# Optimization experiments

Hardware: AMD Instinct MI355X
Metric: run time of the kernel (lower is better)

## Reference

```python
import jax, jax.numpy as jnp
import numpy as np

NUM_EMBEDDINGS = 8192
EMA_DECAY = 0.99


def setup_inputs() -> dict:
    key = jax.random.key(0)
    k1, k2 = jax.random.split(key)
    encodings = jax.random.normal(k1, (16, 128, 32, 32), dtype=jnp.float32)
    weight = 0.02 * jax.random.normal(k2, (NUM_EMBEDDINGS, 128), dtype=jnp.float32)
    return {"encodings": encodings, "weight": weight}


def reference(encodings, weight):
    B, C, H, W = encodings.shape
    K = weight.shape[0]
    # [B, C, H, W] -> [N, C], N = B*H*W
    x = encodings.transpose(0, 2, 3, 1).reshape(-1, C)
    # pairwise squared distances via norms + matmul: [N, K]
    dist = (
        jnp.sum(x * x, axis=1, keepdims=True)
        + jnp.sum(weight * weight, axis=1)[None, :]
        - 2.0 * jnp.matmul(x, weight.T)
    )
    quantized_ids = jnp.argmin(dist, axis=1)  # [N] int
    # straight-through estimator
    q = x + jax.lax.stop_gradient(weight[quantized_ids] - x)  # [N, C]
    # training-mode EMA codebook update (scatter-add counts and sums)
    counts = jax.ops.segment_sum(
        jnp.ones((x.shape[0],), dtype=x.dtype), quantized_ids, num_segments=K
    )
    sums = jax.ops.segment_sum(x, quantized_ids, num_segments=K)
    new_means = sums / (counts[:, None] + 1e-12)
    new_weight = EMA_DECAY * weight + (1.0 - EMA_DECAY) * new_means
    ids_out = quantized_ids.reshape(B, H, W)
    q_out = q.reshape(B, H, W, C).transpose(0, 3, 1, 2)  # [B, C, H, W]
    return ids_out, q_out, new_weight
```

## Files before the change

kernel.cpp:

```cpp
#include <hip/hip_runtime.h>
#include <stdint.h>
#include <stddef.h>


#define N_ROWS   16384
#define K_CODES  8192
#define C_DIM    128

typedef _Float16 f16x8 __attribute__((ext_vector_type(8)));
typedef float    f32x4 __attribute__((ext_vector_type(4)));

__global__ __launch_bounds__(256) void prep(const float* __restrict__ enc,
                                            const float* __restrict__ w,
                                            _Float16* __restrict__ Ap,
                                            _Float16* __restrict__ Bp,
                                            float* __restrict__ xT,
                                            float* __restrict__ xnorm,
                                            float* __restrict__ wnorm,
                                            float* __restrict__ wnmax128) {
  __shared__ float t[128][65];
  const int tid = threadIdx.x;
  if (blockIdx.x < 256) {
    const int b = blockIdx.x >> 4;
    const int hw0 = (blockIdx.x & 15) << 6;
    #pragma unroll
    for (int i = 0; i < 32; ++i) {
      int idx = i * 256 + tid;
      int c = idx >> 6, hwl = idx & 63;
      t[c][hwl] = enc[((size_t)(b * 128 + c) << 10) + hw0 + hwl];
    }
    __syncthreads();
    const int r = tid >> 2, sub = tid & 3;
    const int n = (b << 10) + hw0 + r;
    const int R = n >> 4, m = n & 15;
    float s = 0.f;
    #pragma unroll
    for (int q = 0; q < 4; ++q) {
      f16x8 hv;
      float vv[8];
      #pragma unroll
      for (int e = 0; e < 8; ++e) {
        float v = t[sub * 32 + q * 8 + e][r];
        vv[e] = v;
        s += v * v;
        hv[e] = (_Float16)v;
      }
      *(f16x8*)(Ap + ((size_t)(R * 4 + sub) * 64 + (m + 16 * q)) * 8) = hv;
      *(float4*)(xT + (size_t)n * 128 + sub * 32 + q * 8) =
          (float4){vv[0], vv[1], vv[2], vv[3]};
      *(float4*)(xT + (size_t)n * 128 + sub * 32 + q * 8 + 4) =
          (float4){vv[4], vv[5], vv[6], vv[7]};
    }
    s += __shfl_xor(s, 1);
    s += __shfl_xor(s, 2);
    if (sub == 0) xnorm[n] = s;
  } else {
    __shared__ float wred[4];
    const int kk = (blockIdx.x - 256) * 64 + (tid >> 2), sub = tid & 3;
    const int R = kk >> 4, m = kk & 15;
    const float* base = w + (size_t)kk * C_DIM + sub * 32;
    float s = 0.f;
    #pragma unroll
    for (int q = 0; q < 4; ++q) {
      f16x8 hv;
      float4 va = *(const float4*)(base + q * 8);
      float4 vb = *(const float4*)(base + q * 8 + 4);
      float vv[8] = {va.x, va.y, va.z, va.w, vb.x, vb.y, vb.z, vb.w};
      #pragma unroll
      for (int e = 0; e < 8; ++e) { s += vv[e] * vv[e]; hv[e] = (_Float16)vv[e]; }
      *(f16x8*)(Bp + ((size_t)(R * 4 + sub) * 64 + (m + 16 * q)) * 8) = hv;
    }
    s += __shfl_xor(s, 1);
    s += __shfl_xor(s, 2);
    if (sub == 0) wnorm[kk] = s;
    float wx = s;
    #pragma unroll
    for (int st = 1; st <= 32; st <<= 1) wx = fmaxf(wx, __shfl_xor(wx, st));
    if ((tid & 63) == 0) wred[tid >> 6] = wx;
    __syncthreads();
    if (tid == 0)
      wnmax128[blockIdx.x - 256] =
          fmaxf(fmaxf(wred[0], wred[1]), fmaxf(wred[2], wred[3]));
  }
}

__global__ __launch_bounds__(512) void gemm_argmin(
    const _Float16* __restrict__ Ap, const _Float16* __restrict__ Bp,
    const float* __restrict__ wnorm,
    float* __restrict__ pd1, float* __restrict__ pd2,
    unsigned* __restrict__ icount, unsigned* __restrict__ fcount)
{
  __shared__ _Float16 sbuf[2][16384];
  const int tid = threadIdx.x;
  const int lane = tid & 63, wave = tid >> 6;
  const int m = lane & 15, q = lane >> 4;
  const int cs = blockIdx.x;
  const int row0 = blockIdx.y * 128;
  const int Tr = blockIdx.y * 8 + wave;

  if (cs == 0 && blockIdx.y == 0 && tid == 0) {
    *icount = 0u; *fcount = 0u;
  }

#define STAGE(b, itn) do {                                                   \
    const size_t bh_ = ((size_t)((cs * 64 + (itn) * 8) * 4) << 9);           \
    _Pragma("unroll")                                                        \
    for (int r_ = 0; r_ < 4; ++r_) {                                         \
      __builtin_amdgcn_global_load_lds(                                      \
          (const __attribute__((address_space(1))) void*)                    \
              (Bp + bh_ + ((size_t)(r_ * 512 + tid) << 3)),                  \
          (__attribute__((address_space(3))) void*)                          \
              (&sbuf[b][(r_ * 512 + tid) << 3]),                             \
          16, 0, 0);                                                         \
    }                                                                        \
  } while (0)

  f16x8 bx[4];
  #pragma unroll
  for (int kc = 0; kc < 4; ++kc)
    bx[kc] = *(const f16x8*)(Ap + (((size_t)Tr * 4 + kc) << 9) + (lane << 3));
  const int row = row0 + wave * 16 + m;
  const unsigned q5 = (unsigned)(q << 5);

  STAGE(0, 0);

  for (int it = 0; it < 8; ++it) {
    __syncthreads();
    if (it < 7) STAGE((it + 1) & 1, it + 1);
    const _Float16* fb = &sbuf[it & 1][0];
    const int T0 = cs * 64 + it * 8;
    const int g = cs * 8 + it;
    f32x4 acc[8];
    #pragma unroll
    for (int tj = 0; tj < 8; ++tj) acc[tj] = (f32x4){0.f, 0.f, 0.f, 0.f};
    #pragma unroll
    for (int kc = 0; kc < 4; ++kc) {
      #pragma unroll
      for (int tj = 0; tj < 8; ++tj) {
        f16x8 a = *(const f16x8*)(fb + ((tj * 4 + kc) << 9) + (lane << 3));
        acc[tj] = __builtin_amdgcn_mfma_f32_16x16x32_f16(a, bx[kc], acc[tj], 0, 0, 0);
      }
    }
    float m1t[8], m2t[8];
    #pragma unroll
    for (int tj = 0; tj < 8; ++tj) {
      const int cb = (T0 + tj) * 16 + 4 * q;
      float4 wnq = *(const float4*)(wnorm + cb);
      unsigned b0 = __float_as_uint(fmaf(-2.0f, acc[tj][0], wnq.x)) & 0xFFFFFF80u;
      unsigned b1 = __float_as_uint(fmaf(-2.0f, acc[tj][1], wnq.y)) & 0xFFFFFF80u;
      unsigned b2 = __float_as_uint(fmaf(-2.0f, acc[tj][2], wnq.z)) & 0xFFFFFF80u;
      unsigned b3 = __float_as_uint(fmaf(-2.0f, acc[tj][3], wnq.w)) & 0xFFFFFF80u;
      float v0 = __uint_as_float(b0);
      float v1 = __uint_as_float(b1 | 1u);
      float v2 = __uint_as_float(b2 | 2u);
      float v3 = __uint_as_float(b3 | 3u);
      float l1 = fminf(v0, v1), h1 = fmaxf(v0, v1);
      float l2 = fminf(v2, v3), h2 = fmaxf(v2, v3);
      float mm1 = fminf(l1, l2);
      float mm2 = fminf(fminf(h1, h2), fmaxf(l1, l2));
      m1t[tj] = __uint_as_float(__float_as_uint(mm1) | (unsigned)(tj << 2));
      m2t[tj] = mm2;
    }
    #pragma unroll
    for (int st = 1; st < 8; st <<= 1)
      #pragma unroll
      for (int j = 0; j < 8; j += 2 * st) {
        float a1 = m1t[j], b1 = m1t[j + st];
        m2t[j] = fminf(fminf(m2t[j], m2t[j + st]), fmaxf(a1, b1));
        m1t[j] = fminf(a1, b1);
      }
    float d1 = __uint_as_float(__float_as_uint(m1t[0]) | q5);
    float d2 = m2t[0];
    #pragma unroll
    for (int s = 16; s <= 32; s <<= 1) {
      float o1 = __shfl_xor(d1, s), o2 = __shfl_xor(d2, s);
      d2 = fminf(fminf(d2, o2), fmaxf(d1, o1));
      d1 = fminf(d1, o1);
    }
    if (q == 0) {
      size_t pi = (size_t)g * N_ROWS + row;
      pd1[pi] = d1;
      pd2[pi] = d2;
    }
  }
#undef STAGE
}

__global__ __launch_bounds__(256) void classify(
    const float* __restrict__ pd1, const float* __restrict__ pd2,
    const float* __restrict__ xnorm, const float* __restrict__ wnmax128,
    int* __restrict__ ids, unsigned* __restrict__ items,
    unsigned* __restrict__ icount, int* __restrict__ fulll,
    unsigned* __restrict__ fcount, unsigned long long* __restrict__ keys,
    unsigned* __restrict__ cnt)
{
  __shared__ float wred[4];
  const int tid = threadIdx.x;
  const int gidx = blockIdx.x * 256 + tid;
  const int row = gidx >> 2, p = gidx & 3;
  if (p == 0) keys[row] = ~0ull;
  if (gidx < K_CODES) cnt[gidx] = 0u;
  float wv = wnmax128[tid & 127];
  #pragma unroll
  for (int st = 1; st <= 32; st <<= 1) wv = fmaxf(wv, __shfl_xor(wv, st));
  if ((tid & 63) == 0) wred[tid >> 6] = wv;
  __syncthreads();
  const float wm = fmaxf(fmaxf(wred[0], wred[1]), fmaxf(wred[2], wred[3]));

  float v1[16];
  float lmin = __builtin_inff();
  #pragma unroll
  for (int j = 0; j < 16; ++j) {
    v1[j] = pd1[(size_t)(p * 16 + j) * N_ROWS + row];
    lmin = fminf(lmin, v1[j]);
  }
  lmin = fminf(lmin, __shfl_xor(lmin, 1));
  lmin = fminf(lmin, __shfl_xor(lmin, 2));
  float twoE = 2.0f * (0.0029297f * sqrtf(xnorm[row] * wm) + 5e-4f);
  float T = lmin + twoE;
  bool full = false;
  int nc = 0;
  unsigned cands[6];
  #pragma unroll
  for (int j = 0; j < 16; ++j) {
    size_t i = (size_t)(p * 16 + j) * N_ROWS + row;
    if (pd2[i] <= T) { full = true; }
    else if (v1[j] <= T) {
      if (nc < 6) {
        unsigned ui = __float_as_uint(v1[j]) & 127u;
        unsigned g = (unsigned)(p * 16 + j);
        cands[nc++] = (g << 7) | (((ui >> 2) & 7u) << 4) |
                      ((ui >> 5) << 2) | (ui & 3u);
      } else full = true;
    }
  }
  unsigned fm = full ? 1u : 0u;
  int nct = nc;
  fm |= (unsigned)__shfl_xor((int)fm, 1); nct += __shfl_xor(nct, 1);
  fm |= (unsigned)__shfl_xor((int)fm, 2); nct += __shfl_xor(nct, 2);
  if (nct > 6) fm = 1u;
  if (fm) {
    if (p == 0) { unsigned fi = atomicAdd(fcount, 1u); fulll[fi] = row; }
  } else if (nct >= 2) {
    if (nc > 0) {
      unsigned base = atomicAdd(icount, (unsigned)nc);
      for (int i2 = 0; i2 < nc; ++i2)
        items[base + i2] = ((unsigned)row << 13) | cands[i2];
    }
  } else if (nc == 1) {
    ids[row] = (int)cands[0];
  }
}

__global__ __launch_bounds__(256) void refine(
    const float* __restrict__ xT, const float* __restrict__ w,
    const float* __restrict__ xnorm, const float* __restrict__ wnorm,
    const unsigned* __restrict__ items, const unsigned* __restrict__ icount,
    const int* __restrict__ fulll, const unsigned* __restrict__ fcount,
    unsigned long long* __restrict__ keys) {
  const int tid = threadIdx.x;
  const int lane = tid & 63, wave = tid >> 6;
  const unsigned ic = *icount;
  for (unsigned i = blockIdx.x * 256 + tid; i < ic; i += gridDim.x * 256) {
    unsigned it = items[i];
    int row = (int)(it >> 13), c = (int)(it & 8191u);
    const float* xb = xT + (size_t)row * C_DIM;
    const float* wk = w + (size_t)c * C_DIM;
    float s = 0.f;
    #pragma unroll 8
    for (int c4 = 0; c4 < 32; ++c4) {
      float4 xv = *(const float4*)(xb + c4 * 4);
      float4 wv = *(const float4*)(wk + c4 * 4);
      s = fmaf(xv.x, wv.x, s);
      s = fmaf(xv.y, wv.y, s);
      s = fmaf(xv.z, wv.z, s);
      s = fmaf(xv.w, wv.w, s);
    }
    float d = (xnorm[row] + wnorm[c]) - 2.0f * s;
    unsigned sb = __float_as_uint(d);
    sb = (sb >> 31) ? ~sb : (sb | 0x80000000u);
    unsigned long long key = ((unsigned long long)sb << 32) | (unsigned)c;
    atomicMin(&keys[row], key);
  }
  __shared__ __align__(16) float xs[128];
  __shared__ unsigned long long red[4];
  const unsigned nitems = *fcount * 8;
  for (unsigned item = blockIdx.x; item < nitems; item += gridDim.x) {
    const int row = fulll[item >> 3];
    const int slice = (int)(item & 7u);
    if (tid < 128)
      xs[tid] = xT[(size_t)row * C_DIM + tid];
    __syncthreads();
    const float xn = xnorm[row];
    const int k0 = slice * 1024 + tid * 4;
    float S[4];
    #pragma unroll
    for (int j = 0; j < 4; ++j) S[j] = 0.f;
    for (int c4 = 0; c4 < 32; ++c4) {
      float4 xv = *(const float4*)(&xs[c4 * 4]);
      #pragma unroll
      for (int j = 0; j < 4; ++j) {
        float4 wv = *(const float4*)(w + (size_t)(k0 + j) * C_DIM + c4 * 4);
        S[j] = fmaf(xv.x, wv.x, S[j]);
        S[j] = fmaf(xv.y, wv.y, S[j]);
        S[j] = fmaf(xv.z, wv.z, S[j]);
        S[j] = fmaf(xv.w, wv.w, S[j]);
      }
    }
    unsigned long long best = ~0ull;
    #pragma unroll
    for (int j = 0; j < 4; ++j) {
      float d = (xn + wnorm[k0 + j]) - 2.0f * S[j];
      unsigned sb = __float_as_uint(d);
      sb = (sb >> 31) ? ~sb : (sb | 0x80000000u);
      unsigned long long key = ((unsigned long long)sb << 32) | (unsigned)(k0 + j);
      best = best < key ? best : key;
    }
    #pragma unroll
    for (int s = 1; s <= 32; s <<= 1) {
      unsigned long long ok = __shfl_xor(best, s);
      best = ok < best ? ok : best;
    }
    if (lane == 0) red[wave] = best;
    __syncthreads();
    if (tid == 0) {
      unsigned long long bk = red[0];
      #pragma unroll
      for (int wv = 1; wv < 4; ++wv) bk = red[wv] < bk ? red[wv] : bk;
      atomicMin(&keys[row], bk);
    }
    __syncthreads();
  }
}

__global__ void resolve_ids(const unsigned long long* __restrict__ keys,
                            int* __restrict__ ids, unsigned* __restrict__ cnt,
                            float* __restrict__ out_ids) {
  int row = blockIdx.x * 256 + threadIdx.x;
  unsigned long long k = keys[row];
  int id = (k != ~0ull) ? (int)(unsigned)(k & 0xffffffffu) : ids[row];
  ids[row] = id;
  out_ids[row] = (float)id;
  atomicAdd(&cnt[id], 1u);
}

__global__ __launch_bounds__(256) void scanfill(
    const unsigned* __restrict__ cnt, const int* __restrict__ ids,
    unsigned* __restrict__ offs, int* __restrict__ rowlist) {
  __shared__ unsigned sc[K_CODES];
  __shared__ unsigned tot[256];
  const int tid = threadIdx.x;
  unsigned local[32], run = 0;
  #pragma unroll
  for (int i = 0; i < 32; ++i) { local[i] = run; run += cnt[tid * 32 + i]; }
  tot[tid] = run;
  __syncthreads();
  for (int st = 1; st < 256; st <<= 1) {
    unsigned v = (tid >= st) ? tot[tid - st] : 0u;
    __syncthreads();
    tot[tid] += v;
    __syncthreads();
  }
  unsigned excl = (tid == 0) ? 0u : tot[tid - 1];
  #pragma unroll
  for (int i = 0; i < 32; ++i) {
    unsigned o = excl + local[i];
    offs[tid * 32 + i] = o;
    sc[tid * 32 + i] = o;
  }
  __syncthreads();
  for (int r = tid; r < N_ROWS; r += 256) {
    unsigned slot = atomicAdd(&sc[ids[r]], 1u);
    rowlist[slot] = r;
  }
}

__global__ __launch_bounds__(256) void qsum_final(
    const float* __restrict__ enc, const float* __restrict__ w,
    const int* __restrict__ ids,
    const unsigned* __restrict__ cnt, const unsigned* __restrict__ offs,
    const int* __restrict__ rowlist, const float* __restrict__ xT,
    float* __restrict__ outq, float* __restrict__ outw) {
  if (blockIdx.x < 2048) {
    int e = blockIdx.x * 1024 + threadIdx.x * 4;
    int c = (e >> 10) & 127;
    int b = e >> 17;
    int n = (b << 10) | (e & 1023);
    float4 x = *(const float4*)(enc + e);
    float4 o;
    o.x = x.x + (w[(size_t)ids[n + 0] * C_DIM + c] - x.x);
    o.y = x.y + (w[(size_t)ids[n + 1] * C_DIM + c] - x.y);
    o.z = x.z + (w[(size_t)ids[n + 2] * C_DIM + c] - x.z);
    o.w = x.w + (w[(size_t)ids[n + 3] * C_DIM + c] - x.w);
    *(float4*)(outq + e) = o;
  } else {
    const int tid = threadIdx.x;
    const int lane = tid & 63, wave = tid >> 6;
    const int k = (int)(blockIdx.x - 2048) * 4 + wave;
    const unsigned n0 = offs[k], nk = cnt[k];
    float S0a = 0.f, S0b = 0.f, S0c = 0.f, S0d = 0.f;
    float S1a = 0.f, S1b = 0.f, S1c = 0.f, S1d = 0.f;
    unsigned i = 0;
    for (; i + 4 <= nk; i += 4) {
      int r0 = rowlist[n0 + i],     r1 = rowlist[n0 + i + 1];
      int r2 = rowlist[n0 + i + 2], r3 = rowlist[n0 + i + 3];
      S0a += xT[(size_t)r0 * 128 + lane];      S1a += xT[(size_t)r0 * 128 + lane + 64];
      S0b += xT[(size_t)r1 * 128 + lane];      S1b += xT[(size_t)r1 * 128 + lane + 64];
      S0c += xT[(size_t)r2 * 128 + lane];      S1c += xT[(size_t)r2 * 128 + lane + 64];
      S0d += xT[(size_t)r3 * 128 + lane];      S1d += xT[(size_t)r3 * 128 + lane + 64];
    }
    for (; i < nk; ++i) {
      int r = rowlist[n0 + i];
      S0a += xT[(size_t)r * 128 + lane];
      S1a += xT[(size_t)r * 128 + lane + 64];
    }
    float S0 = (S0a + S0b) + (S0c + S0d);
    float S1 = (S1a + S1b) + (S1c + S1d);
    const float omd = (float)(1.0 - 0.99);
    float cf = (float)nk + 1e-12f;
    outw[(size_t)k * 128 + lane]      = 0.99f * w[(size_t)k * 128 + lane]      + omd * (S0 / cf);
    outw[(size_t)k * 128 + lane + 64] = 0.99f * w[(size_t)k * 128 + lane + 64] + omd * (S1 / cf);
  }
}

extern "C" void kernel_launch(void* const* d_in, const int* in_sizes, int n_in,
                              void* d_out, int out_size, void* d_ws, size_t ws_size,
                              hipStream_t stream) {
  const float* enc = (const float*)d_in[0];
  const float* w   = (const float*)d_in[1];
  float* out = (float*)d_out;
  float* out_ids = out;
  float* out_q   = out + N_ROWS;
  float* out_w   = out + N_ROWS + N_ROWS * C_DIM;

  char* ws = (char*)d_ws;
  _Float16* Ap  = (_Float16*)(ws);
  _Float16* Bp  = (_Float16*)(ws + 4194304);
  float* xnorm  = (float*)(ws + 6291456);
  float* wnorm  = (float*)(ws + 6356992);
  float* pd1    = (float*)(ws + 6389760);
  float* pd2    = (float*)(ws + 10584064);
  float* wnmax128 = (float*)(ws + 14778368);
  int* ids      = (int*)(ws + 18972672);
  int* fulll    = (int*)(ws + 19038208);
  unsigned* items = (unsigned*)(ws + 19103744);
  unsigned* icount = (unsigned*)(ws + 20152324);
  unsigned* fcount = (unsigned*)(ws + 20152328);
  unsigned* cnt    = (unsigned*)(ws + 20152336);
  unsigned* offs   = (unsigned*)(ws + 20185104);
  unsigned long long* keys = (unsigned long long*)(ws + 20250640);
  int* rowlist  = (int*)(ws + 20381712);
  float* xT     = (float*)(ws + 20447248);
  (void)in_sizes; (void)n_in; (void)out_size; (void)ws_size;


  prep<<<384, 256, 0, stream>>>(enc, w, Ap, Bp, xT, xnorm, wnorm, wnmax128);
  gemm_argmin<<<dim3(8, N_ROWS / 128), 512, 0, stream>>>(
      Ap, Bp, wnorm, pd1, pd2, icount, fcount);
  classify<<<N_ROWS * 4 / 256, 256, 0, stream>>>(
      pd1, pd2, xnorm, wnmax128, ids, items, icount, fulll, fcount, keys, cnt);
  refine<<<2048, 256, 0, stream>>>(xT, w, xnorm, wnorm, items, icount, fulll,
                                   fcount, keys);
  resolve_ids<<<N_ROWS / 256, 256, 0, stream>>>(keys, ids, cnt, out_ids);
  scanfill<<<1, 256, 0, stream>>>(cnt, ids, offs, rowlist);
  qsum_final<<<2048 + K_CODES / 4, 256, 0, stream>>>(
      enc, w, ids, cnt, offs, rowlist, xT, out_q, out_w);
}
```

Measured before the change: 229.5 us.

## Halve GEMM LDS tile with half-group pipeline and parallelize rowlist fill

The GEMM-argmin kernel now stages 4 codebook tiles per pipeline step instead of 8, cutting its LDS buffer in half (64KB to 32KB). It carries running top-2 minima across pairs of half-groups so the partial outputs stay the same. The aim is higher occupancy and smaller register pressure, at the cost of twice as many barriers and staging steps. Separately, the single-block scanfill is split into a scan kernel and a grid-wide fill_rowlist kernel. The fill step then runs its atomics on global memory across many blocks rather than on LDS in one block.

```diff
diff --git a/kernel.cpp b/kernel.cpp
--- a/kernel.cpp
+++ b/kernel.cpp
@@ -90,7 +90,7 @@
     float* __restrict__ pd1, float* __restrict__ pd2,
     unsigned* __restrict__ icount, unsigned* __restrict__ fcount)
 {
-  __shared__ _Float16 sbuf[2][16384];
+  __shared__ _Float16 sbuf[2][8192];
   const int tid = threadIdx.x;
   const int lane = tid & 63, wave = tid >> 6;
   const int m = lane & 15, q = lane >> 4;
@@ -102,10 +102,10 @@
     *icount = 0u; *fcount = 0u;
   }
 
-#define STAGE(b, itn) do {                                                   \
-    const size_t bh_ = ((size_t)((cs * 64 + (itn) * 8) * 4) << 9);           \
+#define STAGE(b, hgn) do {                                                   \
+    const size_t bh_ = ((size_t)((cs * 64 + (hgn) * 4) * 4) << 9);           \
     _Pragma("unroll")                                                        \
-    for (int r_ = 0; r_ < 4; ++r_) {                                         \
+    for (int r_ = 0; r_ < 2; ++r_) {                                         \
       __builtin_amdgcn_global_load_lds(                                      \
           (const __attribute__((address_space(1))) void*)                    \
               (Bp + bh_ + ((size_t)(r_ * 512 + tid) << 3)),                  \
@@ -124,32 +124,33 @@
 
   STAGE(0, 0);
 
-  for (int it = 0; it < 8; ++it) {
-    __syncthreads();
-    if (it < 7) STAGE((it + 1) & 1, it + 1);
-    const _Float16* fb = &sbuf[it & 1][0];
-    const int T0 = cs * 64 + it * 8;
-    const int g = cs * 8 + it;
-    f32x4 acc[8];
-    #pragma unroll
-    for (int tj = 0; tj < 8; ++tj) acc[tj] = (f32x4){0.f, 0.f, 0.f, 0.f};
+  float c1 = 0.f, c2 = 0.f;
+  for (int hg = 0; hg < 16; ++hg) {
+    __syncthreads();
+    if (hg < 15) STAGE((hg + 1) & 1, hg + 1);
+    const _Float16* fb = &sbuf[hg & 1][0];
+    const int half = hg & 1;
+    f32x4 acc[4];
+    #pragma unroll
+    for (int t = 0; t < 4; ++t) acc[t] = (f32x4){0.f, 0.f, 0.f, 0.f};
     #pragma unroll
     for (int kc = 0; kc < 4; ++kc) {
       #pragma unroll
-      for (int tj = 0; tj < 8; ++tj) {
-        f16x8 a = *(const f16x8*)(fb + ((tj * 4 + kc) << 9) + (lane << 3));
-        acc[tj] = __builtin_amdgcn_mfma_f32_16x16x32_f16(a, bx[kc], acc[tj], 0, 0, 0);
+      for (int t = 0; t < 4; ++t) {
+        f16x8 a = *(const f16x8*)(fb + ((t * 4 + kc) << 9) + (lane << 3));
+        acc[t] = __builtin_amdgcn_mfma_f32_16x16x32_f16(a, bx[kc], acc[t], 0, 0, 0);
       }
     }
-    float m1t[8], m2t[8];
-    #pragma unroll
-    for (int tj = 0; tj < 8; ++tj) {
-      const int cb = (T0 + tj) * 16 + 4 * q;
+    float m1t[4], m2t[4];
+    #pragma unroll
+    for (int t = 0; t < 4; ++t) {
+      const int tj = half * 4 + t;
+      const int cb = (cs * 64 + hg * 4 + t) * 16 + 4 * q;
       float4 wnq = *(const float4*)(wnorm + cb);
-      unsigned b0 = __float_as_uint(fmaf(-2.0f, acc[tj][0], wnq.x)) & 0xFFFFFF80u;
-      unsigned b1 = __float_as_uint(fmaf(-2.0f, acc[tj][1], wnq.y)) & 0xFFFFFF80u;
-      unsigned b2 = __float_as_uint(fmaf(-2.0f, acc[tj][2], wnq.z)) & 0xFFFFFF80u;
-      unsigned b3 = __float_as_uint(fmaf(-2.0f, acc[tj][3], wnq.w)) & 0xFFFFFF80u;
+      unsigned b0 = __float_as_uint(fmaf(-2.0f, acc[t][0], wnq.x)) & 0xFFFFFF80u;
+      unsigned b1 = __float_as_uint(fmaf(-2.0f, acc[t][1], wnq.y)) & 0xFFFFFF80u;
+      unsigned b2 = __float_as_uint(fmaf(-2.0f, acc[t][2], wnq.z)) & 0xFFFFFF80u;
+      unsigned b3 = __float_as_uint(fmaf(-2.0f, acc[t][3], wnq.w)) & 0xFFFFFF80u;
       float v0 = __uint_as_float(b0);
       float v1 = __uint_as_float(b1 | 1u);
       float v2 = __uint_as_float(b2 | 2u);
@@ -158,29 +159,34 @@
       float l2 = fminf(v2, v3), h2 = fmaxf(v2, v3);
       float mm1 = fminf(l1, l2);
       float mm2 = fminf(fminf(h1, h2), fmaxf(l1, l2));
-      m1t[tj] = __uint_as_float(__float_as_uint(mm1) | (unsigned)(tj << 2));
-      m2t[tj] = mm2;
-    }
-    #pragma unroll
-    for (int st = 1; st < 8; st <<= 1)
-      #pragma unroll
-      for (int j = 0; j < 8; j += 2 * st) {
-        float a1 = m1t[j], b1 = m1t[j + st];
-        m2t[j] = fminf(fminf(m2t[j], m2t[j + st]), fmaxf(a1, b1));
-        m1t[j] = fminf(a1, b1);
+      m1t[t] = __uint_as_float(__float_as_uint(mm1) | (unsigned)(tj << 2));
+      m2t[t] = mm2;
+    }
+    m2t[0] = fminf(fminf(m2t[0], m2t[1]), fmaxf(m1t[0], m1t[1]));
+    m1t[0] = fminf(m1t[0], m1t[1]);
+    m2t[2] = fminf(fminf(m2t[2], m2t[3]), fmaxf(m1t[2], m1t[3]));
+    m1t[2] = fminf(m1t[2], m1t[3]);
+    m2t[0] = fminf(fminf(m2t[0], m2t[2]), fmaxf(m1t[0], m1t[2]));
+    m1t[0] = fminf(m1t[0], m1t[2]);
+    if (half == 0) {
+      c1 = m1t[0]; c2 = m2t[0];
+    } else {
+      c2 = fminf(fminf(c2, m2t[0]), fmaxf(c1, m1t[0]));
+      c1 = fminf(c1, m1t[0]);
+      float d1 = __uint_as_float(__float_as_uint(c1) | q5);
+      float d2 = c2;
+      #pragma unroll
+      for (int s = 16; s <= 32; s <<= 1) {
+        float o1 = __shfl_xor(d1, s), o2 = __shfl_xor(d2, s);
+        d2 = fminf(fminf(d2, o2), fmaxf(d1, o1));
+        d1 = fminf(d1, o1);
       }
-    float d1 = __uint_as_float(__float_as_uint(m1t[0]) | q5);
-    float d2 = m2t[0];
-    #pragma unroll
-    for (int s = 16; s <= 32; s <<= 1) {
-      float o1 = __shfl_xor(d1, s), o2 = __shfl_xor(d2, s);
-      d2 = fminf(fminf(d2, o2), fmaxf(d1, o1));
-      d1 = fminf(d1, o1);
-    }
-    if (q == 0) {
-      size_t pi = (size_t)g * N_ROWS + row;
-      pd1[pi] = d1;
-      pd2[pi] = d2;
+      if (q == 0) {
+        const int g = cs * 8 + (hg >> 1);
+        size_t pi = (size_t)g * N_ROWS + row;
+        pd1[pi] = d1;
+        pd2[pi] = d2;
+      }
     }
   }
 #undef STAGE
@@ -344,10 +350,9 @@
   atomicAdd(&cnt[id], 1u);
 }
 
-__global__ __launch_bounds__(256) void scanfill(
-    const unsigned* __restrict__ cnt, const int* __restrict__ ids,
-    unsigned* __restrict__ offs, int* __restrict__ rowlist) {
-  __shared__ unsigned sc[K_CODES];
+__global__ __launch_bounds__(256) void scan_offsets(
+    const unsigned* __restrict__ cnt,
+    unsigned* __restrict__ offs, unsigned* __restrict__ cursor) {
   __shared__ unsigned tot[256];
   const int tid = threadIdx.x;
   unsigned local[32], run = 0;
@@ -366,13 +371,16 @@
   for (int i = 0; i < 32; ++i) {
     unsigned o = excl + local[i];
     offs[tid * 32 + i] = o;
-    sc[tid * 32 + i] = o;
-  }
-  __syncthreads();
-  for (int r = tid; r < N_ROWS; r += 256) {
-    unsigned slot = atomicAdd(&sc[ids[r]], 1u);
-    rowlist[slot] = r;
-  }
+    cursor[tid * 32 + i] = o;
+  }
+}
+
+__global__ void fill_rowlist(const int* __restrict__ ids,
+                             unsigned* __restrict__ cursor,
+                             int* __restrict__ rowlist) {
+  int row = blockIdx.x * 256 + threadIdx.x;
+  unsigned slot = atomicAdd(&cursor[ids[row]], 1u);
+  rowlist[slot] = row;
 }
 
 __global__ __launch_bounds__(256) void qsum_final(
@@ -448,6 +456,7 @@
   unsigned* fcount = (unsigned*)(ws + 20152328);
   unsigned* cnt    = (unsigned*)(ws + 20152336);
   unsigned* offs   = (unsigned*)(ws + 20185104);
+  unsigned* cursor = (unsigned*)(ws + 20217872);
   unsigned long long* keys = (unsigned long long*)(ws + 20250640);
   int* rowlist  = (int*)(ws + 20381712);
   float* xT     = (float*)(ws + 20447248);
@@ -462,7 +471,8 @@
   refine<<<2048, 256, 0, stream>>>(xT, w, xnorm, wnorm, items, icount, fulll,
                                    fcount, keys);
   resolve_ids<<<N_ROWS / 256, 256, 0, stream>>>(keys, ids, cnt, out_ids);
-  scanfill<<<1, 256, 0, stream>>>(cnt, ids, offs, rowlist);
+  scan_offsets<<<1, 256, 0, stream>>>(cnt, offs, cursor);
+  fill_rowlist<<<N_ROWS / 256, 256, 0, stream>>>(ids, cursor, rowlist);
   qsum_final<<<2048 + K_CODES / 4, 256, 0, stream>>>(
       enc, w, ids, cnt, offs, rowlist, xT, out_q, out_w);
 }
```

Result: faster. 207.8 us (-9.4%).
